# Performance work log

Measured on AMD Instinct MI355X. Metric: run time of the kernel, lower is better.

Reference implementation:

```python
import jax, jax.numpy as jnp
import numpy as np

N = 250_000   # nodes per graph batch
E = 4_000_000 # edges
G = 1024      # graphs (segments)
F_IN, C, D = 6, 64, 5
EPS = 1e-5    # PyG LayerNorm eps


def setup_inputs() -> dict:
    key = jax.random.key(0)
    ks = jax.random.split(key, 30)
    rn = lambda k, s: jax.random.normal(k, s, jnp.float32)
    p = lambda k, s: rn(k, s) * 0.05
    return {
        "x1": rn(ks[0], (N, F_IN)),
        "edge_index1": jax.random.randint(ks[1], (2, E), 0, N, jnp.int32),
        "batch1": jnp.sort(jax.random.randint(ks[2], (N,), 0, G, jnp.int32)),
        "x2": rn(ks[3], (N, F_IN)),
        "edge_index2": jax.random.randint(ks[4], (2, E), 0, N, jnp.int32),
        "batch2": jnp.sort(jax.random.randint(ks[5], (N,), 0, G, jnp.int32)),
        "d1": rn(ks[6], (G, D)),
        "d2": rn(ks[7], (G, D)),
        # GIN MLP 1: Linear(6,64) -> ReLU -> Linear(64,64)
        "W1": p(ks[8], (F_IN, C)), "b1": jnp.zeros((C,), jnp.float32),
        "W2": p(ks[9], (C, C)),    "b2": jnp.zeros((C,), jnp.float32),
        "ln1w": jnp.ones((C,), jnp.float32), "ln1b": jnp.zeros((C,), jnp.float32),
        # GIN MLP 2
        "W3": p(ks[10], (C, C)), "b3": jnp.zeros((C,), jnp.float32),
        "W4": p(ks[11], (C, C)), "b4": jnp.zeros((C,), jnp.float32),
        "ln2w": jnp.ones((C,), jnp.float32), "ln2b": jnp.zeros((C,), jnp.float32),
        # head: Linear(138,128) -> Linear(128,64) -> Linear(64,1)
        "Wf1": p(ks[12], (2 * C + 2 * D, 128)), "bf1": jnp.zeros((128,), jnp.float32),
        "Wf2": p(ks[13], (128, 64)),            "bf2": jnp.zeros((64,), jnp.float32),
        "Wo": p(ks[14], (64, 1)),               "bo": jnp.zeros((1,), jnp.float32),
    }


def _gin(x, src, dst, Wa, ba, Wb, bb):
    # GINConv, eps=0: h = x + sum_{j in N(i)} x_j ; then MLP (dropout = eval identity)
    agg = jax.ops.segment_sum(x[src], dst, num_segments=N)
    h = x + agg
    h = jax.nn.relu(h @ Wa + ba)
    return h @ Wb + bb


def _graph_layernorm(x, batch, w, b):
    # PyG LayerNorm mode='graph': normalize over all nodes AND channels per graph
    cnt = jax.ops.segment_sum(jnp.ones((x.shape[0],), x.dtype), batch, num_segments=G)
    norm = jnp.maximum(cnt, 1.0) * x.shape[-1]          # [G]
    mean = jax.ops.segment_sum(x.sum(-1), batch, num_segments=G) / norm
    xc = x - mean[batch][:, None]
    var = jax.ops.segment_sum((xc * xc).sum(-1), batch, num_segments=G) / norm
    out = xc * jax.lax.rsqrt(var + EPS)[batch][:, None]
    return out * w + b


def _forward_one(x, edge_index, batch, W1, b1, W2, b2, ln1w, ln1b, W3, b3, W4, b4, ln2w, ln2b):
    src, dst = edge_index[0], edge_index[1]
    x = jax.nn.relu(_graph_layernorm(_gin(x, src, dst, W1, b1, W2, b2), batch, ln1w, ln1b))
    x = jax.nn.relu(_graph_layernorm(_gin(x, src, dst, W3, b3, W4, b4), batch, ln2w, ln2b))
    add = jax.ops.segment_sum(x, batch, num_segments=G)  # [G, C]
    cnt = jax.ops.segment_sum(jnp.ones((x.shape[0],), x.dtype), batch, num_segments=G)
    mean = add / jnp.maximum(cnt, 1.0)[:, None]
    return add + mean


def reference(x1, edge_index1, batch1, x2, edge_index2, batch2, d1, d2,
              W1, b1, W2, b2, ln1w, ln1b, W3, b3, W4, b4, ln2w, ln2b,
              Wf1, bf1, Wf2, bf2, Wo, bo):
    shared = (W1, b1, W2, b2, ln1w, ln1b, W3, b3, W4, b4, ln2w, ln2b)
    emb1 = _forward_one(x1, edge_index1, batch1, *shared)
    emb2 = _forward_one(x2, edge_index2, batch2, *shared)
    h = jnp.concatenate([emb1, emb2, d1, d2], axis=1)    # [G, 138]
    h = jax.nn.relu(h @ Wf1 + bf1)                       # dropout identity (eval)
    h = jax.nn.relu(h @ Wf2 + bf2)
    return h @ Wo + bo                                   # [G, 1]
```

## Files before the change

### kernel.cpp

```cpp
#include <hip/hip_runtime.h>

typedef unsigned short ushort_t;
typedef __attribute__((ext_vector_type(8))) short bf16x8;
typedef __attribute__((ext_vector_type(4))) float f32x4;

#define FIN 6
#define CAP 20480

__device__ __forceinline__ float blo(unsigned u) { return __uint_as_float(u << 16); }
__device__ __forceinline__ float bhi(unsigned u) { return __uint_as_float(u & 0xffff0000u); }
__device__ __forceinline__ ushort_t f2b(float f) {
  unsigned u = __float_as_uint(f);
  unsigned r = (u + 0x7fffu + ((u >> 16) & 1u)) >> 16;
  return (ushort_t)r;
}
__device__ __forceinline__ float b2f(ushort_t s) { return __uint_as_float(((unsigned)s) << 16); }
__device__ __forceinline__ unsigned pk2(float lo, float hi) {
  return ((unsigned)f2b(hi) << 16) | (unsigned)f2b(lo);
}
union U4F { uint4 u; bf16x8 v; };
__device__ __forceinline__ bf16x8 asfrag(uint4 u) { U4F x; x.u = u; return x.v; }

#define EPT 32
#define TILE 8192

__global__ void k_binit(int* __restrict__ ecur, int* __restrict__ off, int nbuk, int N, int E) {
  int t = threadIdx.x;
  if (t < nbuk) ecur[t] = t * CAP;
  if (t == 0) off[N] = E;
}

__global__ __launch_bounds__(256) void k_bscatter(const int* __restrict__ src,
    const int* __restrict__ dst, int* __restrict__ ecur,
    unsigned* __restrict__ ebuf, int E, int nbuk) {
  __shared__ int cnt[256];
  __shared__ int gbase[256];
  int t = threadIdx.x;
  cnt[t] = 0;
  __syncthreads();
  int base = blockIdx.x * TILE;
  unsigned pk[EPT];
  unsigned pv[EPT];
  #pragma unroll
  for (int k = 0; k < EPT; ++k) {
    int e = base + k * 256 + t;
    if (e < E) {
      int d = dst[e];
      int b = d >> 10;
      int r = atomicAdd(&cnt[b], 1);
      pk[k] = (unsigned)b | ((unsigned)r << 8);
      pv[k] = ((unsigned)(d & 1023) << 18) | (unsigned)src[e];
    } else {
      pk[k] = 0xFFFFFFFFu;
    }
  }
  __syncthreads();
  if (t < nbuk && cnt[t] > 0) gbase[t] = atomicAdd(&ecur[t], cnt[t]);
  __syncthreads();
  #pragma unroll
  for (int k = 0; k < EPT; ++k) {
    if (pk[k] != 0xFFFFFFFFu) {
      int b = pk[k] & 255;
      int r = pk[k] >> 8;
      ebuf[gbase[b] + r] = pv[k];
    }
  }
}

__global__ __launch_bounds__(256) void k_bscan2(const int* __restrict__ ecur,
    int* __restrict__ ebase, int nbuk) {
  __shared__ int lds[256];
  int t = threadIdx.x;
  int s = (t < nbuk) ? (ecur[t] - t * CAP) : 0;
  lds[t] = s; __syncthreads();
  int acc = s;
  for (int o = 1; o < 256; o <<= 1) {
    int add = (t >= o) ? lds[t - o] : 0;
    __syncthreads();
    acc += add; lds[t] = acc;
    __syncthreads();
  }
  if (t < nbuk) ebase[t] = acc - s;
}

__global__ __launch_bounds__(256) void k_bcsr(const unsigned* __restrict__ ebuf,
    const int* __restrict__ ecur, const int* __restrict__ ebase,
    int* __restrict__ off, int* __restrict__ csr, int N) {
  __shared__ int hist[1024];
  __shared__ int lofs[1024];
  __shared__ int sc[256];
  int b = blockIdx.x, t = threadIdx.x;
  int nb0 = b << 10;
  int bn = N - nb0; if (bn > 1024) bn = 1024;
  int s_beg = b * CAP, s_end = ecur[b];
  int base = ebase[b];
  #pragma unroll
  for (int k = 0; k < 4; ++k) hist[t * 4 + k] = 0;
  __syncthreads();
  for (int e = s_beg + t; e < s_end; e += 256) atomicAdd(&hist[ebuf[e] >> 18], 1);
  __syncthreads();
  int h0 = hist[t * 4 + 0], h1 = hist[t * 4 + 1], h2 = hist[t * 4 + 2], h3 = hist[t * 4 + 3];
  int s = h0 + h1 + h2 + h3;
  sc[t] = s; __syncthreads();
  int acc = s;
  for (int o = 1; o < 256; o <<= 1) {
    int add = (t >= o) ? sc[t - o] : 0;
    __syncthreads();
    acc += add; sc[t] = acc;
    __syncthreads();
  }
  int run = acc - s;
  lofs[t * 4 + 0] = run; run += h0;
  lofs[t * 4 + 1] = run; run += h1;
  lofs[t * 4 + 2] = run; run += h2;
  lofs[t * 4 + 3] = run;
  __syncthreads();
  #pragma unroll
  for (int k = 0; k < 4; ++k) {
    int j = t * 4 + k;
    if (j < bn) off[nb0 + j] = base + lofs[j];
  }
  __syncthreads();
  for (int e = s_beg + t; e < s_end; e += 256) {
    unsigned p = ebuf[e];
    int r = atomicAdd(&lofs[p >> 18], 1);
    csr[base + r] = (int)(p & 0x3FFFFu);
  }
}

__global__ void k_bounds(const int* __restrict__ batch, int* __restrict__ gstart, int n, int G) {
  int i = blockIdx.x * 256 + threadIdx.x;
  if (i >= n) return;
  int b = batch[i];
  if (i == 0) { for (int g = 0; g <= b; ++g) gstart[g] = 0; }
  else { int pb = batch[i - 1]; for (int g = pb + 1; g <= b; ++g) gstart[g] = i; }
  if (i == n - 1) { for (int g = b + 1; g <= G; ++g) gstart[g] = n; }
}

__global__ void k_xpack(const float* __restrict__ x, unsigned* __restrict__ xb, int n) {
  int tt = blockIdx.x * 256 + threadIdx.x;
  if (tt >= n * 4) return;
  int i = tt >> 2, k = tt & 3;
  unsigned v = 0;
  if (k < 3) {
    float2 f = *(const float2*)(x + (size_t)i * 6 + k * 2);
    v = pk2(f.x, f.y);
  }
  xb[tt] = v;
}

__global__ void k_wpack(const float* __restrict__ W2, const float* __restrict__ W3,
                        const float* __restrict__ W4, uint4* __restrict__ wfrag) {
  int idx = blockIdx.x * 256 + threadIdx.x;
  if (idx >= 3 * 512) return;
  int widx = idx >> 9, rem = idx & 511;
  int mt = rem >> 7, kh = (rem >> 6) & 1, l = rem & 63;
  int g = l >> 4, c = l & 15;
  const float* W = (widx == 0) ? W2 : (widx == 1) ? W3 : W4;
  int k0 = kh * 32 + g * 8;
  int col = mt * 16 + c;
  uint4 v;
  v.x = pk2(W[(k0 + 0) * 64 + col], W[(k0 + 1) * 64 + col]);
  v.y = pk2(W[(k0 + 2) * 64 + col], W[(k0 + 3) * 64 + col]);
  v.z = pk2(W[(k0 + 4) * 64 + col], W[(k0 + 5) * 64 + col]);
  v.w = pk2(W[(k0 + 6) * 64 + col], W[(k0 + 7) * 64 + col]);
  wfrag[idx] = v;
}

#define ACC6(u) { a0 += blo(u.x); a1 += bhi(u.x); a2 += blo(u.y); a3 += bhi(u.y); a4 += blo(u.z); a5 += bhi(u.z); }
__global__ __launch_bounds__(256) void k_gin1a(const uint4* __restrict__ xb4,
    const int* __restrict__ off, const int* __restrict__ csr,
    const float* __restrict__ W1, const float* __restrict__ b1,
    ushort_t* __restrict__ t1, int n) {
  int t = threadIdx.x, w = t >> 6, lane = t & 63;
  int nd = lane >> 3, sl = lane & 7;
  int i = blockIdx.x * 32 + w * 8 + nd;

  float w1r[FIN];
  #pragma unroll
  for (int k = 0; k < FIN; ++k) w1r[k] = W1[k * 64 + lane];
  float bb1 = b1[lane];

  float a0 = 0, a1 = 0, a2 = 0, a3 = 0, a4 = 0, a5 = 0;
  if (i < n) {
    int e0 = off[i], e1 = off[i + 1];
    int e = e0 + sl;
    for (; e + 8 < e1; e += 16) {
      uint4 u = xb4[csr[e]];
      uint4 v = xb4[csr[e + 8]];
      ACC6(u); ACC6(v);
    }
    if (e < e1) { uint4 u = xb4[csr[e]]; ACC6(u); }
    if (sl == 0) { uint4 u = xb4[i]; ACC6(u); }
  }
  #pragma unroll
  for (int m = 1; m < 8; m <<= 1) {
    a0 += __shfl_xor(a0, m); a1 += __shfl_xor(a1, m); a2 += __shfl_xor(a2, m);
    a3 += __shfl_xor(a3, m); a4 += __shfl_xor(a4, m); a5 += __shfl_xor(a5, m);
  }
  __shared__ float sh[4][8][FIN];
  if (sl < FIN) {
    float v = (sl == 0) ? a0 : (sl == 1) ? a1 : (sl == 2) ? a2 : (sl == 3) ? a3 : (sl == 4) ? a4 : a5;
    sh[w][nd][sl] = v;
  }
  #pragma unroll
  for (int nd2 = 0; nd2 < 8; ++nd2) {
    int node = blockIdx.x * 32 + w * 8 + nd2;
    if (node >= n) break;
    float h = bb1;
    #pragma unroll
    for (int k = 0; k < FIN; ++k) h = fmaf(sh[w][nd2][k], w1r[k], h);
    t1[(size_t)node * 64 + lane] = f2b(fmaxf(h, 0.f));
  }
}

__global__ __launch_bounds__(256) void k_lin_mfma(const ushort_t* __restrict__ in,
    const uint4* __restrict__ wf, const float* __restrict__ bias,
    ushort_t* __restrict__ out, int n) {
  __shared__ __align__(16) ushort_t lds[4][16][72];
  int t = threadIdx.x, w = t >> 6, l = t & 63;
  int g = l >> 4, c = l & 15;
  bf16x8 af[4][2];
  #pragma unroll
  for (int mt = 0; mt < 4; ++mt)
    #pragma unroll
    for (int kh = 0; kh < 2; ++kh) af[mt][kh] = asfrag(wf[(mt * 2 + kh) * 64 + l]);
  float bs[4][4];
  #pragma unroll
  for (int mt = 0; mt < 4; ++mt)
    #pragma unroll
    for (int r = 0; r < 4; ++r) bs[mt][r] = bias[mt * 16 + 4 * g + r];

  int ntile = (n + 15) >> 4;
  for (int tau = blockIdx.x * 4 + w; tau < ntile; tau += gridDim.x * 4) {
    int nb = tau << 4;
    int row = nb + c; if (row >= n) row = n - 1;
    const uint4* rp = (const uint4*)(in + (size_t)row * 64);
    bf16x8 bf0 = asfrag(rp[g]);
    bf16x8 bf1 = asfrag(rp[g + 4]);
    f32x4 acc[4];
    #pragma unroll
    for (int mt = 0; mt < 4; ++mt) {
      acc[mt] = (f32x4){bs[mt][0], bs[mt][1], bs[mt][2], bs[mt][3]};
      acc[mt] = __builtin_amdgcn_mfma_f32_16x16x32_bf16(af[mt][0], bf0, acc[mt], 0, 0, 0);
      acc[mt] = __builtin_amdgcn_mfma_f32_16x16x32_bf16(af[mt][1], bf1, acc[mt], 0, 0, 0);
    }
    #pragma unroll
    for (int mt = 0; mt < 4; ++mt) {
      uint2 pv;
      pv.x = pk2(acc[mt][0], acc[mt][1]);
      pv.y = pk2(acc[mt][2], acc[mt][3]);
      *(uint2*)&lds[w][c][mt * 16 + 4 * g] = pv;
    }
    int n2 = l >> 2, ch = (l & 3) * 16;
    uint4 s0 = *(const uint4*)&lds[w][n2][ch];
    uint4 s1 = *(const uint4*)&lds[w][n2][ch + 8];
    int orow = nb + n2;
    if (orow < n) {
      uint4* op = (uint4*)(out + (size_t)orow * 64);
      op[(l & 3) * 2] = s0;
      op[(l & 3) * 2 + 1] = s1;
    }
  }
}

__global__ __launch_bounds__(256) void k_mlp2_mfma(const ushort_t* __restrict__ aggb,
    const uint4* __restrict__ wf3, const float* __restrict__ b3,
    const uint4* __restrict__ wf4, const float* __restrict__ b4,
    ushort_t* __restrict__ zb, int n) {
  __shared__ __align__(16) ushort_t lds[4][16][72];
  int t = threadIdx.x, w = t >> 6, l = t & 63;
  int g = l >> 4, c = l & 15;
  bf16x8 a3[4][2], a4[4][2];
  #pragma unroll
  for (int mt = 0; mt < 4; ++mt)
    #pragma unroll
    for (int kh = 0; kh < 2; ++kh) {
      a3[mt][kh] = asfrag(wf3[(mt * 2 + kh) * 64 + l]);
      a4[mt][kh] = asfrag(wf4[(mt * 2 + kh) * 64 + l]);
    }
  float bs3[4][4], bs4[4][4];
  #pragma unroll
  for (int mt = 0; mt < 4; ++mt)
    #pragma unroll
    for (int r = 0; r < 4; ++r) {
      bs3[mt][r] = b3[mt * 16 + 4 * g + r];
      bs4[mt][r] = b4[mt * 16 + 4 * g + r];
    }

  int ntile = (n + 15) >> 4;
  for (int tau = blockIdx.x * 4 + w; tau < ntile; tau += gridDim.x * 4) {
    int nb = tau << 4;
    int row = nb + c; if (row >= n) row = n - 1;
    const uint4* rp = (const uint4*)(aggb + (size_t)row * 64);
    bf16x8 bf0 = asfrag(rp[g]);
    bf16x8 bf1 = asfrag(rp[g + 4]);
    f32x4 acc[4];
    #pragma unroll
    for (int mt = 0; mt < 4; ++mt) {
      acc[mt] = (f32x4){bs3[mt][0], bs3[mt][1], bs3[mt][2], bs3[mt][3]};
      acc[mt] = __builtin_amdgcn_mfma_f32_16x16x32_bf16(a3[mt][0], bf0, acc[mt], 0, 0, 0);
      acc[mt] = __builtin_amdgcn_mfma_f32_16x16x32_bf16(a3[mt][1], bf1, acc[mt], 0, 0, 0);
    }
    #pragma unroll
    for (int mt = 0; mt < 4; ++mt) {
      uint2 pv;
      pv.x = pk2(fmaxf(acc[mt][0], 0.f), fmaxf(acc[mt][1], 0.f));
      pv.y = pk2(fmaxf(acc[mt][2], 0.f), fmaxf(acc[mt][3], 0.f));
      *(uint2*)&lds[w][c][mt * 16 + 4 * g] = pv;
    }
    bf16x8 h0 = asfrag(*(const uint4*)&lds[w][c][8 * g]);
    bf16x8 h1 = asfrag(*(const uint4*)&lds[w][c][8 * g + 32]);
    f32x4 ac2[4];
    #pragma unroll
    for (int mt = 0; mt < 4; ++mt) {
      ac2[mt] = (f32x4){bs4[mt][0], bs4[mt][1], bs4[mt][2], bs4[mt][3]};
      ac2[mt] = __builtin_amdgcn_mfma_f32_16x16x32_bf16(a4[mt][0], h0, ac2[mt], 0, 0, 0);
      ac2[mt] = __builtin_amdgcn_mfma_f32_16x16x32_bf16(a4[mt][1], h1, ac2[mt], 0, 0, 0);
    }
    #pragma unroll
    for (int mt = 0; mt < 4; ++mt) {
      uint2 pv;
      pv.x = pk2(ac2[mt][0], ac2[mt][1]);
      pv.y = pk2(ac2[mt][2], ac2[mt][3]);
      *(uint2*)&lds[w][c][mt * 16 + 4 * g] = pv;
    }
    int n2 = l >> 2, ch = (l & 3) * 16;
    uint4 s0 = *(const uint4*)&lds[w][n2][ch];
    uint4 s1 = *(const uint4*)&lds[w][n2][ch + 8];
    int orow = nb + n2;
    if (orow < n) {
      uint4* op = (uint4*)(zb + (size_t)orow * 64);
      op[(l & 3) * 2] = s0;
      op[(l & 3) * 2 + 1] = s1;
    }
  }
}

#define ACC8(u) { a0 += blo(u.x); a1 += bhi(u.x); a2 += blo(u.y); a3 += bhi(u.y); \
                  a4 += blo(u.z); a5 += bhi(u.z); a6 += blo(u.w); a7 += bhi(u.w); }
__global__ __launch_bounds__(256) void k_agg64(const ushort_t* __restrict__ hb,
    const int* __restrict__ off, const int* __restrict__ csr,
    ushort_t* __restrict__ aggb, int n) {
  int t = threadIdx.x, w = t >> 6, lane = t & 63;
  int i = blockIdx.x * 4 + w;
  if (i >= n) return;
  int grp = lane >> 3, sl = lane & 7;
  int e0 = off[i], e1 = off[i + 1];
  const uint4* hb4 = (const uint4*)hb;
  float a0 = 0, a1 = 0, a2 = 0, a3 = 0, a4 = 0, a5 = 0, a6 = 0, a7 = 0;
  int e = e0 + grp;
  for (; e + 8 < e1; e += 16) {
    int sa = csr[e], sb = csr[e + 8];
    uint4 ua = hb4[(size_t)sa * 8 + sl];
    uint4 ub = hb4[(size_t)sb * 8 + sl];
    ACC8(ua); ACC8(ub);
  }
  if (e < e1) {
    int sa = csr[e];
    uint4 ua = hb4[(size_t)sa * 8 + sl];
    ACC8(ua);
  }
  #pragma unroll
  for (int m = 8; m < 64; m <<= 1) {
    a0 += __shfl_xor(a0, m); a1 += __shfl_xor(a1, m); a2 += __shfl_xor(a2, m);
    a3 += __shfl_xor(a3, m); a4 += __shfl_xor(a4, m); a5 += __shfl_xor(a5, m);
    a6 += __shfl_xor(a6, m); a7 += __shfl_xor(a7, m);
  }
  if (grp == 0) {
    uint4 us = hb4[(size_t)i * 8 + sl];
    ACC8(us);
    uint4 o;
    o.x = pk2(a0, a1); o.y = pk2(a2, a3); o.z = pk2(a4, a5); o.w = pk2(a6, a7);
    ((uint4*)aggb)[(size_t)i * 8 + sl] = o;
  }
}

__global__ __launch_bounds__(256) void k_ln_statsb(const ushort_t* __restrict__ h,
    const int* __restrict__ gstart, float* __restrict__ gmean, float* __restrict__ ginv) {
  int g = blockIdx.x;
  int s0 = gstart[g], s1 = gstart[g + 1];
  const uint2* p2 = (const uint2*)h;
  size_t j0 = (size_t)s0 * 16, j1 = (size_t)s1 * 16;
  float s = 0.f, ss = 0.f;
  for (size_t j = j0 + threadIdx.x; j < j1; j += 256) {
    uint2 u = p2[j];
    float v0 = blo(u.x), v1 = bhi(u.x), v2 = blo(u.y), v3 = bhi(u.y);
    s += (v0 + v1) + (v2 + v3);
    ss += v0 * v0 + v1 * v1 + v2 * v2 + v3 * v3;
  }
  __shared__ float l1[256], l2[256];
  l1[threadIdx.x] = s; l2[threadIdx.x] = ss;
  __syncthreads();
  for (int o = 128; o > 0; o >>= 1) {
    if (threadIdx.x < o) { l1[threadIdx.x] += l1[threadIdx.x + o]; l2[threadIdx.x] += l2[threadIdx.x + o]; }
    __syncthreads();
  }
  if (threadIdx.x == 0) {
    float cnt = (float)(s1 - s0);
    float norm = fmaxf(cnt, 1.f) * 64.f;
    float mean = l1[0] / norm;
    float var = l2[0] / norm - mean * mean;
    var = fmaxf(var, 0.f);
    gmean[g] = mean;
    ginv[g] = rsqrtf(var + 1e-5f);
  }
}

__global__ void k_ln_apply_relu(const ushort_t* __restrict__ hr, const int* __restrict__ batch,
    const float* __restrict__ gmean, const float* __restrict__ ginv,
    const float* __restrict__ w, const float* __restrict__ bb,
    ushort_t* __restrict__ hb, int n) {
  int tt = blockIdx.x * 256 + threadIdx.x;
  if (tt >= n * 8) return;
  int i = tt >> 3, q = tt & 7;
  int g = batch[i];
  float mean = gmean[g], inv = ginv[g];
  uint4 u = ((const uint4*)hr)[tt];
  float4 w0 = *(const float4*)(w + q * 8);
  float4 w1 = *(const float4*)(w + q * 8 + 4);
  float4 c0 = *(const float4*)(bb + q * 8);
  float4 c1 = *(const float4*)(bb + q * 8 + 4);
  uint4 o;
  o.x = pk2(fmaxf((blo(u.x) - mean) * inv * w0.x + c0.x, 0.f),
            fmaxf((bhi(u.x) - mean) * inv * w0.y + c0.y, 0.f));
  o.y = pk2(fmaxf((blo(u.y) - mean) * inv * w0.z + c0.z, 0.f),
            fmaxf((bhi(u.y) - mean) * inv * w0.w + c0.w, 0.f));
  o.z = pk2(fmaxf((blo(u.z) - mean) * inv * w1.x + c1.x, 0.f),
            fmaxf((bhi(u.z) - mean) * inv * w1.y + c1.y, 0.f));
  o.w = pk2(fmaxf((blo(u.w) - mean) * inv * w1.z + c1.z, 0.f),
            fmaxf((bhi(u.w) - mean) * inv * w1.w + c1.w, 0.f));
  ((uint4*)hb)[tt] = o;
}

__global__ __launch_bounds__(256) void k_pool(const ushort_t* __restrict__ zb,
    const int* __restrict__ gstart, const float* __restrict__ gmean, const float* __restrict__ ginv,
    const float* __restrict__ w, const float* __restrict__ bb, float* __restrict__ emb) {
  int g = blockIdx.x;
  int s0 = gstart[g], s1 = gstart[g + 1];
  int t = threadIdx.x, c2 = t & 31, sub = t >> 5;
  float mean = gmean[g], inv = ginv[g];
  float w0 = w[c2 * 2], w1 = w[c2 * 2 + 1], b0 = bb[c2 * 2], b1v = bb[c2 * 2 + 1];
  float acc0 = 0.f, acc1 = 0.f;
  const unsigned* zp = (const unsigned*)zb;
  for (int i = s0 + sub; i < s1; i += 8) {
    unsigned u = zp[(size_t)i * 32 + c2];
    acc0 += fmaxf((blo(u) - mean) * inv * w0 + b0, 0.f);
    acc1 += fmaxf((bhi(u) - mean) * inv * w1 + b1v, 0.f);
  }
  __shared__ float l0[256], l1[256];
  l0[t] = acc0; l1[t] = acc1;
  __syncthreads();
  if (sub == 0) {
    float t0 = 0.f, t1v = 0.f;
    #pragma unroll
    for (int s = 0; s < 8; ++s) { t0 += l0[s * 32 + c2]; t1v += l1[s * 32 + c2]; }
    float cnt = fmaxf((float)(s1 - s0), 1.f);
    emb[g * 64 + c2 * 2]     = t0 + t0 / cnt;
    emb[g * 64 + c2 * 2 + 1] = t1v + t1v / cnt;
  }
}

__global__ __launch_bounds__(128) void k_head(const float* __restrict__ emb1,
    const float* __restrict__ emb2, const float* __restrict__ d1, const float* __restrict__ d2,
    const float* __restrict__ Wf1, const float* __restrict__ bf1,
    const float* __restrict__ Wf2, const float* __restrict__ bf2,
    const float* __restrict__ Wo, const float* __restrict__ bo, float* __restrict__ out) {
  int g = blockIdx.x, t = threadIdx.x;
  __shared__ float v[138], h1s[128], h2s[64];
  if (t < 64) v[t] = emb1[g * 64 + t];
  else v[t] = emb2[g * 64 + (t - 64)];
  if (t < 5) v[128 + t] = d1[g * 5 + t];
  else if (t < 10) v[133 + (t - 5)] = d2[g * 5 + (t - 5)];
  __syncthreads();
  float a = bf1[t];
  for (int k = 0; k < 138; ++k) a = fmaf(v[k], Wf1[k * 128 + t], a);
  h1s[t] = fmaxf(a, 0.f);
  __syncthreads();
  if (t < 64) {
    float a2 = bf2[t];
    #pragma unroll 8
    for (int k = 0; k < 128; ++k) a2 = fmaf(h1s[k], Wf2[k * 64 + t], a2);
    h2s[t] = fmaxf(a2, 0.f);
  }
  __syncthreads();
  if (t == 0) {
    float s = bo[0];
    for (int k = 0; k < 64; ++k) s += h2s[k] * Wo[k];
    out[g] = s;
  }
}

extern "C" void kernel_launch(void* const* d_in, const int* in_sizes, int n_in,
                              void* d_out, int out_size, void* d_ws, size_t ws_size,
                              hipStream_t stream) {
  const float* x1     = (const float*)d_in[0];
  const int*   ei1    = (const int*)d_in[1];
  const int*   batch1 = (const int*)d_in[2];
  const float* x2     = (const float*)d_in[3];
  const int*   ei2    = (const int*)d_in[4];
  const int*   batch2 = (const int*)d_in[5];
  const float* d1     = (const float*)d_in[6];
  const float* d2     = (const float*)d_in[7];
  const float* W1  = (const float*)d_in[8],  *b1  = (const float*)d_in[9];
  const float* W2  = (const float*)d_in[10], *b2  = (const float*)d_in[11];
  const float* ln1w = (const float*)d_in[12], *ln1b = (const float*)d_in[13];
  const float* W3  = (const float*)d_in[14], *b3  = (const float*)d_in[15];
  const float* W4  = (const float*)d_in[16], *b4  = (const float*)d_in[17];
  const float* ln2w = (const float*)d_in[18], *ln2b = (const float*)d_in[19];
  const float* Wf1 = (const float*)d_in[20], *bf1 = (const float*)d_in[21];
  const float* Wf2 = (const float*)d_in[22], *bf2 = (const float*)d_in[23];
  const float* Wo  = (const float*)d_in[24], *bo  = (const float*)d_in[25];
  float* out = (float*)d_out;

  const int N = in_sizes[0] / FIN;
  const int G = in_sizes[6] / 5;
  const int E1 = in_sizes[1] / 2;
  const int E2 = in_sizes[4] / 2;
  const int Emax = (E1 > E2) ? E1 : E2;
  const int NBUK = (N + 1023) >> 10;

  char* p = (char*)d_ws;
  auto alloc = [&](size_t bytes) { void* r = p; p += (bytes + 255) & ~(size_t)255; return r; };
  int*      off    = (int*)alloc((size_t)(N + 1) * 4);
  int*      ecur   = (int*)alloc(256 * 4);
  int*      ebase  = (int*)alloc(257 * 4);
  int*      csr    = (int*)alloc((size_t)Emax * 4);
  int*      gstart = (int*)alloc((size_t)(G + 1) * 4);
  float*    gmean  = (float*)alloc((size_t)G * 4);
  float*    ginv   = (float*)alloc((size_t)G * 4);
  uint4*    wfrag  = (uint4*)alloc(3 * 512 * 16);
  unsigned* xb     = (unsigned*)alloc((size_t)N * 16);
  ushort_t* t1     = (ushort_t*)alloc((size_t)N * 64 * 2);
  ushort_t* hr     = (ushort_t*)alloc((size_t)N * 64 * 2);
  ushort_t* hb     = (ushort_t*)alloc((size_t)N * 64 * 2);
  float*    emb1   = (float*)alloc((size_t)G * 64 * 4);
  float*    emb2   = (float*)alloc((size_t)G * 64 * 4);
  ushort_t* aggb = t1;
  ushort_t* zb   = hr;
  unsigned* ebuf = (unsigned*)t1;

  const uint4* wf2 = wfrag;
  const uint4* wf3 = wfrag + 512;
  const uint4* wf4 = wfrag + 1024;

  const int GRID_N  = (N + 255) / 256;
  const int GRID_W  = (N + 3) / 4;
  const int GRID_G1 = (N + 31) / 32;
  const int GRID_A  = (N * 8 + 255) / 256;
  const int GRID_P  = (N * 4 + 255) / 256;

  k_wpack<<<6, 256, 0, stream>>>(W2, W3, W4, wfrag);

  auto run_graph = [&](const float* x, const int* ei, const int* batch, int E, float* emb) {
    const int* src = ei;
    const int* dst = ei + E;
    const int SCAT = (E + TILE - 1) / TILE;
    k_binit<<<1, 256, 0, stream>>>(ecur, off, NBUK, N, E);
    k_bscatter<<<SCAT, 256, 0, stream>>>(src, dst, ecur, ebuf, E, NBUK);
    k_bscan2<<<1, 256, 0, stream>>>(ecur, ebase, NBUK);
    k_bcsr<<<NBUK, 256, 0, stream>>>(ebuf, ecur, ebase, off, csr, N);
    k_bounds<<<GRID_N, 256, 0, stream>>>(batch, gstart, N, G);
    k_xpack<<<GRID_P, 256, 0, stream>>>(x, xb, N);

    k_gin1a<<<GRID_G1, 256, 0, stream>>>((const uint4*)xb, off, csr, W1, b1, t1, N);
    k_lin_mfma<<<2048, 256, 0, stream>>>(t1, wf2, b2, hr, N);
    k_ln_statsb<<<G, 256, 0, stream>>>(hr, gstart, gmean, ginv);
    k_ln_apply_relu<<<GRID_A, 256, 0, stream>>>(hr, batch, gmean, ginv, ln1w, ln1b, hb, N);
    k_agg64<<<GRID_W, 256, 0, stream>>>(hb, off, csr, aggb, N);
    k_mlp2_mfma<<<2048, 256, 0, stream>>>(aggb, wf3, b3, wf4, b4, zb, N);
    k_ln_statsb<<<G, 256, 0, stream>>>(zb, gstart, gmean, ginv);
    k_pool<<<G, 256, 0, stream>>>(zb, gstart, gmean, ginv, ln2w, ln2b, emb);
  };

  run_graph(x1, ei1, batch1, E1, emb1);
  run_graph(x2, ei2, batch2, E2, emb2);
  k_head<<<G, 128, 0, stream>>>(emb1, emb2, d1, d2, Wf1, bf1, Wf2, bf2, Wo, bo, out);
}
```

Baseline: 653.0 us.

## Fuse GIN first MLP, graph LayerNorm stats/apply, and pooling into fewer kernels

Merges the bounds and x-packing kernels, fuses the first GIN aggregation and its ReLU linear with the second linear via an LDS tile, and folds LayerNorm statistics together with the normalize pass (and with pooling for the second layer) into per-graph kernels that cache the graph's rows in LDS. This removes intermediate global round trips and several launches per graph. The per-graph LN kernels rely on graphs fitting LNCAP nodes in shared memory, fall back to global reloads otherwise, and use large LDS footprints that may reduce occupancy.

```diff
diff --git a/kernel.cpp b/kernel.cpp
--- a/kernel.cpp
+++ b/kernel.cpp
@@ -6,6 +6,7 @@
 
 #define FIN 6
 #define CAP 20480
+#define LNCAP 384
 
 __device__ __forceinline__ float blo(unsigned u) { return __uint_as_float(u << 16); }
 __device__ __forceinline__ float bhi(unsigned u) { return __uint_as_float(u & 0xffff0000u); }
@@ -128,25 +129,24 @@
   }
 }
 
-__global__ void k_bounds(const int* __restrict__ batch, int* __restrict__ gstart, int n, int G) {
-  int i = blockIdx.x * 256 + threadIdx.x;
-  if (i >= n) return;
-  int b = batch[i];
-  if (i == 0) { for (int g = 0; g <= b; ++g) gstart[g] = 0; }
-  else { int pb = batch[i - 1]; for (int g = pb + 1; g <= b; ++g) gstart[g] = i; }
-  if (i == n - 1) { for (int g = b + 1; g <= G; ++g) gstart[g] = n; }
-}
-
-__global__ void k_xpack(const float* __restrict__ x, unsigned* __restrict__ xb, int n) {
+__global__ void k_prep(const float* __restrict__ x, const int* __restrict__ batch,
+                       unsigned* __restrict__ xb, int* __restrict__ gstart, int n, int G) {
   int tt = blockIdx.x * 256 + threadIdx.x;
-  if (tt >= n * 4) return;
-  int i = tt >> 2, k = tt & 3;
-  unsigned v = 0;
-  if (k < 3) {
-    float2 f = *(const float2*)(x + (size_t)i * 6 + k * 2);
-    v = pk2(f.x, f.y);
-  }
-  xb[tt] = v;
+  if (tt < n * 4) {
+    int i = tt >> 2, k = tt & 3;
+    unsigned v = 0;
+    if (k < 3) {
+      float2 f = *(const float2*)(x + (size_t)i * 6 + k * 2);
+      v = pk2(f.x, f.y);
+    }
+    xb[tt] = v;
+  }
+  if (tt < n) {
+    int b = batch[tt];
+    if (tt == 0) { for (int g = 0; g <= b; ++g) gstart[g] = 0; }
+    else { int pb = batch[tt - 1]; for (int g = pb + 1; g <= b; ++g) gstart[g] = tt; }
+    if (tt == n - 1) { for (int g = b + 1; g <= G; ++g) gstart[g] = n; }
+  }
 }
 
 __global__ void k_wpack(const float* __restrict__ W2, const float* __restrict__ W3,
@@ -168,13 +168,17 @@
 }
 
 #define ACC6(u) { a0 += blo(u.x); a1 += bhi(u.x); a2 += blo(u.y); a3 += bhi(u.y); a4 += blo(u.z); a5 += bhi(u.z); }
-__global__ __launch_bounds__(256) void k_gin1a(const uint4* __restrict__ xb4,
+__global__ __launch_bounds__(256) void k_gin1f(const uint4* __restrict__ xb4,
     const int* __restrict__ off, const int* __restrict__ csr,
     const float* __restrict__ W1, const float* __restrict__ b1,
-    ushort_t* __restrict__ t1, int n) {
+    const uint4* __restrict__ wf2, const float* __restrict__ b2,
+    ushort_t* __restrict__ hr, int n) {
+  __shared__ __align__(16) ushort_t t1s[32][72];
+  __shared__ float sh[4][8][FIN];
   int t = threadIdx.x, w = t >> 6, lane = t & 63;
   int nd = lane >> 3, sl = lane & 7;
-  int i = blockIdx.x * 32 + w * 8 + nd;
+  int nb0 = blockIdx.x * 32;
+  int i = nb0 + w * 8 + nd;
 
   float w1r[FIN];
   #pragma unroll
@@ -198,50 +202,33 @@
     a0 += __shfl_xor(a0, m); a1 += __shfl_xor(a1, m); a2 += __shfl_xor(a2, m);
     a3 += __shfl_xor(a3, m); a4 += __shfl_xor(a4, m); a5 += __shfl_xor(a5, m);
   }
-  __shared__ float sh[4][8][FIN];
   if (sl < FIN) {
     float v = (sl == 0) ? a0 : (sl == 1) ? a1 : (sl == 2) ? a2 : (sl == 3) ? a3 : (sl == 4) ? a4 : a5;
     sh[w][nd][sl] = v;
   }
   #pragma unroll
   for (int nd2 = 0; nd2 < 8; ++nd2) {
-    int node = blockIdx.x * 32 + w * 8 + nd2;
-    if (node >= n) break;
     float h = bb1;
     #pragma unroll
     for (int k = 0; k < FIN; ++k) h = fmaf(sh[w][nd2][k], w1r[k], h);
-    t1[(size_t)node * 64 + lane] = f2b(fmaxf(h, 0.f));
-  }
-}
-
-__global__ __launch_bounds__(256) void k_lin_mfma(const ushort_t* __restrict__ in,
-    const uint4* __restrict__ wf, const float* __restrict__ bias,
-    ushort_t* __restrict__ out, int n) {
-  __shared__ __align__(16) ushort_t lds[4][16][72];
-  int t = threadIdx.x, w = t >> 6, l = t & 63;
-  int g = l >> 4, c = l & 15;
-  bf16x8 af[4][2];
-  #pragma unroll
-  for (int mt = 0; mt < 4; ++mt)
-    #pragma unroll
-    for (int kh = 0; kh < 2; ++kh) af[mt][kh] = asfrag(wf[(mt * 2 + kh) * 64 + l]);
-  float bs[4][4];
-  #pragma unroll
-  for (int mt = 0; mt < 4; ++mt)
-    #pragma unroll
-    for (int r = 0; r < 4; ++r) bs[mt][r] = bias[mt * 16 + 4 * g + r];
-
-  int ntile = (n + 15) >> 4;
-  for (int tau = blockIdx.x * 4 + w; tau < ntile; tau += gridDim.x * 4) {
-    int nb = tau << 4;
-    int row = nb + c; if (row >= n) row = n - 1;
-    const uint4* rp = (const uint4*)(in + (size_t)row * 64);
-    bf16x8 bf0 = asfrag(rp[g]);
-    bf16x8 bf1 = asfrag(rp[g + 4]);
+    t1s[w * 8 + nd2][lane] = f2b(fmaxf(h, 0.f));
+  }
+  __syncthreads();
+  if (w < 2) {
+    int g = lane >> 4, c = lane & 15;
+    bf16x8 af[4][2];
+    #pragma unroll
+    for (int mt = 0; mt < 4; ++mt)
+      #pragma unroll
+      for (int kh = 0; kh < 2; ++kh) af[mt][kh] = asfrag(wf2[(mt * 2 + kh) * 64 + lane]);
+    int r0 = w * 16 + c;
+    bf16x8 bf0 = asfrag(*(const uint4*)&t1s[r0][8 * g]);
+    bf16x8 bf1 = asfrag(*(const uint4*)&t1s[r0][8 * g + 32]);
     f32x4 acc[4];
     #pragma unroll
     for (int mt = 0; mt < 4; ++mt) {
-      acc[mt] = (f32x4){bs[mt][0], bs[mt][1], bs[mt][2], bs[mt][3]};
+      acc[mt] = (f32x4){b2[mt * 16 + 4 * g + 0], b2[mt * 16 + 4 * g + 1],
+                        b2[mt * 16 + 4 * g + 2], b2[mt * 16 + 4 * g + 3]};
       acc[mt] = __builtin_amdgcn_mfma_f32_16x16x32_bf16(af[mt][0], bf0, acc[mt], 0, 0, 0);
       acc[mt] = __builtin_amdgcn_mfma_f32_16x16x32_bf16(af[mt][1], bf1, acc[mt], 0, 0, 0);
     }
@@ -250,89 +237,16 @@
       uint2 pv;
       pv.x = pk2(acc[mt][0], acc[mt][1]);
       pv.y = pk2(acc[mt][2], acc[mt][3]);
-      *(uint2*)&lds[w][c][mt * 16 + 4 * g] = pv;
-    }
-    int n2 = l >> 2, ch = (l & 3) * 16;
-    uint4 s0 = *(const uint4*)&lds[w][n2][ch];
-    uint4 s1 = *(const uint4*)&lds[w][n2][ch + 8];
-    int orow = nb + n2;
+      *(uint2*)&t1s[r0][mt * 16 + 4 * g] = pv;
+    }
+    int n2 = lane >> 2, ch = (lane & 3) * 16;
+    uint4 s0 = *(const uint4*)&t1s[w * 16 + n2][ch];
+    uint4 s1 = *(const uint4*)&t1s[w * 16 + n2][ch + 8];
+    int orow = nb0 + w * 16 + n2;
     if (orow < n) {
-      uint4* op = (uint4*)(out + (size_t)orow * 64);
-      op[(l & 3) * 2] = s0;
-      op[(l & 3) * 2 + 1] = s1;
-    }
-  }
-}
-
-__global__ __launch_bounds__(256) void k_mlp2_mfma(const ushort_t* __restrict__ aggb,
-    const uint4* __restrict__ wf3, const float* __restrict__ b3,
-    const uint4* __restrict__ wf4, const float* __restrict__ b4,
-    ushort_t* __restrict__ zb, int n) {
-  __shared__ __align__(16) ushort_t lds[4][16][72];
-  int t = threadIdx.x, w = t >> 6, l = t & 63;
-  int g = l >> 4, c = l & 15;
-  bf16x8 a3[4][2], a4[4][2];
-  #pragma unroll
-  for (int mt = 0; mt < 4; ++mt)
-    #pragma unroll
-    for (int kh = 0; kh < 2; ++kh) {
-      a3[mt][kh] = asfrag(wf3[(mt * 2 + kh) * 64 + l]);
-      a4[mt][kh] = asfrag(wf4[(mt * 2 + kh) * 64 + l]);
-    }
-  float bs3[4][4], bs4[4][4];
-  #pragma unroll
-  for (int mt = 0; mt < 4; ++mt)
-    #pragma unroll
-    for (int r = 0; r < 4; ++r) {
-      bs3[mt][r] = b3[mt * 16 + 4 * g + r];
-      bs4[mt][r] = b4[mt * 16 + 4 * g + r];
-    }
-
-  int ntile = (n + 15) >> 4;
-  for (int tau = blockIdx.x * 4 + w; tau < ntile; tau += gridDim.x * 4) {
-    int nb = tau << 4;
-    int row = nb + c; if (row >= n) row = n - 1;
-    const uint4* rp = (const uint4*)(aggb + (size_t)row * 64);
-    bf16x8 bf0 = asfrag(rp[g]);
-    bf16x8 bf1 = asfrag(rp[g + 4]);
-    f32x4 acc[4];
-    #pragma unroll
-    for (int mt = 0; mt < 4; ++mt) {
-      acc[mt] = (f32x4){bs3[mt][0], bs3[mt][1], bs3[mt][2], bs3[mt][3]};
-      acc[mt] = __builtin_amdgcn_mfma_f32_16x16x32_bf16(a3[mt][0], bf0, acc[mt], 0, 0, 0);
-      acc[mt] = __builtin_amdgcn_mfma_f32_16x16x32_bf16(a3[mt][1], bf1, acc[mt], 0, 0, 0);
-    }
-    #pragma unroll
-    for (int mt = 0; mt < 4; ++mt) {
-      uint2 pv;
-      pv.x = pk2(fmaxf(acc[mt][0], 0.f), fmaxf(acc[mt][1], 0.f));
-      pv.y = pk2(fmaxf(acc[mt][2], 0.f), fmaxf(acc[mt][3], 0.f));
-      *(uint2*)&lds[w][c][mt * 16 + 4 * g] = pv;
-    }
-    bf16x8 h0 = asfrag(*(const uint4*)&lds[w][c][8 * g]);
-    bf16x8 h1 = asfrag(*(const uint4*)&lds[w][c][8 * g + 32]);
-    f32x4 ac2[4];
-    #pragma unroll
-    for (int mt = 0; mt < 4; ++mt) {
-      ac2[mt] = (f32x4){bs4[mt][0], bs4[mt][1], bs4[mt][2], bs4[mt][3]};
-      ac2[mt] = __builtin_amdgcn_mfma_f32_16x16x32_bf16(a4[mt][0], h0, ac2[mt], 0, 0, 0);
-      ac2[mt] = __builtin_amdgcn_mfma_f32_16x16x32_bf16(a4[mt][1], h1, ac2[mt], 0, 0, 0);
-    }
-    #pragma unroll
-    for (int mt = 0; mt < 4; ++mt) {
-      uint2 pv;
-      pv.x = pk2(ac2[mt][0], ac2[mt][1]);
-      pv.y = pk2(ac2[mt][2], ac2[mt][3]);
-      *(uint2*)&lds[w][c][mt * 16 + 4 * g] = pv;
-    }
-    int n2 = l >> 2, ch = (l & 3) * 16;
-    uint4 s0 = *(const uint4*)&lds[w][n2][ch];
-    uint4 s1 = *(const uint4*)&lds[w][n2][ch + 8];
-    int orow = nb + n2;
-    if (orow < n) {
-      uint4* op = (uint4*)(zb + (size_t)orow * 64);
-      op[(l & 3) * 2] = s0;
-      op[(l & 3) * 2 + 1] = s1;
+      uint4* op = (uint4*)(hr + (size_t)orow * 64);
+      op[(lane & 3) * 2] = s0;
+      op[(lane & 3) * 2 + 1] = s1;
     }
   }
 }
@@ -376,88 +290,186 @@
   }
 }
 
-__global__ __launch_bounds__(256) void k_ln_statsb(const ushort_t* __restrict__ h,
-    const int* __restrict__ gstart, float* __restrict__ gmean, float* __restrict__ ginv) {
-  int g = blockIdx.x;
-  int s0 = gstart[g], s1 = gstart[g + 1];
-  const uint2* p2 = (const uint2*)h;
-  size_t j0 = (size_t)s0 * 16, j1 = (size_t)s1 * 16;
+__global__ __launch_bounds__(256) void k_mlp2_mfma(const ushort_t* __restrict__ aggb,
+    const uint4* __restrict__ wf3, const float* __restrict__ b3,
+    const uint4* __restrict__ wf4, const float* __restrict__ b4,
+    ushort_t* __restrict__ zb, int n) {
+  __shared__ __align__(16) ushort_t lds[4][16][72];
+  int t = threadIdx.x, w = t >> 6, l = t & 63;
+  int g = l >> 4, c = l & 15;
+  bf16x8 a3[4][2], a4[4][2];
+  #pragma unroll
+  for (int mt = 0; mt < 4; ++mt)
+    #pragma unroll
+    for (int kh = 0; kh < 2; ++kh) {
+      a3[mt][kh] = asfrag(wf3[(mt * 2 + kh) * 64 + l]);
+      a4[mt][kh] = asfrag(wf4[(mt * 2 + kh) * 64 + l]);
+    }
+  float bs3[4][4], bs4[4][4];
+  #pragma unroll
+  for (int mt = 0; mt < 4; ++mt)
+    #pragma unroll
+    for (int r = 0; r < 4; ++r) {
+      bs3[mt][r] = b3[mt * 16 + 4 * g + r];
+      bs4[mt][r] = b4[mt * 16 + 4 * g + r];
+    }
+  int ntile = (n + 15) >> 4;
+  for (int tau = blockIdx.x * 4 + w; tau < ntile; tau += gridDim.x * 4) {
+    int nb = tau << 4;
+    int row = nb + c; if (row >= n) row = n - 1;
+    const uint4* rp = (const uint4*)(aggb + (size_t)row * 64);
+    bf16x8 bf0 = asfrag(rp[g]);
+    bf16x8 bf1 = asfrag(rp[g + 4]);
+    f32x4 acc[4];
+    #pragma unroll
+    for (int mt = 0; mt < 4; ++mt) {
+      acc[mt] = (f32x4){bs3[mt][0], bs3[mt][1], bs3[mt][2], bs3[mt][3]};
+      acc[mt] = __builtin_amdgcn_mfma_f32_16x16x32_bf16(a3[mt][0], bf0, acc[mt], 0, 0, 0);
+      acc[mt] = __builtin_amdgcn_mfma_f32_16x16x32_bf16(a3[mt][1], bf1, acc[mt], 0, 0, 0);
+    }
+    #pragma unroll
+    for (int mt = 0; mt < 4; ++mt) {
+      uint2 pv;
+      pv.x = pk2(fmaxf(acc[mt][0], 0.f), fmaxf(acc[mt][1], 0.f));
+      pv.y = pk2(fmaxf(acc[mt][2], 0.f), fmaxf(acc[mt][3], 0.f));
+      *(uint2*)&lds[w][c][mt * 16 + 4 * g] = pv;
+    }
+    bf16x8 h0 = asfrag(*(const uint4*)&lds[w][c][8 * g]);
+    bf16x8 h1 = asfrag(*(const uint4*)&lds[w][c][8 * g + 32]);
+    f32x4 ac2[4];
+    #pragma unroll
+    for (int mt = 0; mt < 4; ++mt) {
+      ac2[mt] = (f32x4){bs4[mt][0], bs4[mt][1], bs4[mt][2], bs4[mt][3]};
+      ac2[mt] = __builtin_amdgcn_mfma_f32_16x16x32_bf16(a4[mt][0], h0, ac2[mt], 0, 0, 0);
+      ac2[mt] = __builtin_amdgcn_mfma_f32_16x16x32_bf16(a4[mt][1], h1, ac2[mt], 0, 0, 0);
+    }
+    #pragma unroll
+    for (int mt = 0; mt < 4; ++mt) {
+      uint2 pv;
+      pv.x = pk2(ac2[mt][0], ac2[mt][1]);
+      pv.y = pk2(ac2[mt][2], ac2[mt][3]);
+      *(uint2*)&lds[w][c][mt * 16 + 4 * g] = pv;
+    }
+    int n2 = l >> 2, ch = (l & 3) * 16;
+    uint4 s0 = *(const uint4*)&lds[w][n2][ch];
+    uint4 s1 = *(const uint4*)&lds[w][n2][ch + 8];
+    int orow = nb + n2;
+    if (orow < n) {
+      uint4* op = (uint4*)(zb + (size_t)orow * 64);
+      op[(l & 3) * 2] = s0;
+      op[(l & 3) * 2 + 1] = s1;
+    }
+  }
+}
+
+__global__ __launch_bounds__(256) void k_ln1(const ushort_t* __restrict__ hr,
+    const int* __restrict__ gstart, const float* __restrict__ w, const float* __restrict__ bb,
+    ushort_t* __restrict__ hb) {
+  __shared__ uint4 st[LNCAP * 8];
+  __shared__ float l1[256], l2[256];
+  __shared__ float mm[2];
+  int g = blockIdx.x, t = threadIdx.x;
+  int s0 = gstart[g], s1 = gstart[g + 1], cnt = s1 - s0;
+  const uint4* src = (const uint4*)hr + (size_t)s0 * 8;
+  int nch = cnt * 8;
+  bool fit = cnt <= LNCAP;
   float s = 0.f, ss = 0.f;
-  for (size_t j = j0 + threadIdx.x; j < j1; j += 256) {
-    uint2 u = p2[j];
+  for (int j = t; j < nch; j += 256) {
+    uint4 u = src[j];
+    if (fit) st[j] = u;
     float v0 = blo(u.x), v1 = bhi(u.x), v2 = blo(u.y), v3 = bhi(u.y);
-    s += (v0 + v1) + (v2 + v3);
-    ss += v0 * v0 + v1 * v1 + v2 * v2 + v3 * v3;
-  }
+    float v4 = blo(u.z), v5 = bhi(u.z), v6 = blo(u.w), v7 = bhi(u.w);
+    s += ((v0 + v1) + (v2 + v3)) + ((v4 + v5) + (v6 + v7));
+    ss += ((v0 * v0 + v1 * v1) + (v2 * v2 + v3 * v3)) + ((v4 * v4 + v5 * v5) + (v6 * v6 + v7 * v7));
+  }
+  l1[t] = s; l2[t] = ss;
+  __syncthreads();
+  for (int o = 128; o > 0; o >>= 1) {
+    if (t < o) { l1[t] += l1[t + o]; l2[t] += l2[t + o]; }
+    __syncthreads();
+  }
+  if (t == 0) {
+    float cf = (float)cnt;
+    float norm = fmaxf(cf, 1.f) * 64.f;
+    float mean = l1[0] / norm;
+    float var = fmaxf(l2[0] / norm - mean * mean, 0.f);
+    mm[0] = mean; mm[1] = rsqrtf(var + 1e-5f);
+  }
+  __syncthreads();
+  float mean = mm[0], inv = mm[1];
+  uint4* dst = (uint4*)hb + (size_t)s0 * 8;
+  for (int j = t; j < nch; j += 256) {
+    uint4 u = fit ? st[j] : src[j];
+    int q = j & 7;
+    float4 w0 = *(const float4*)(w + q * 8);
+    float4 w1 = *(const float4*)(w + q * 8 + 4);
+    float4 c0 = *(const float4*)(bb + q * 8);
+    float4 c1 = *(const float4*)(bb + q * 8 + 4);
+    uint4 o;
+    o.x = pk2(fmaxf((blo(u.x) - mean) * inv * w0.x + c0.x, 0.f),
+              fmaxf((bhi(u.x) - mean) * inv * w0.y + c0.y, 0.f));
+    o.y = pk2(fmaxf((blo(u.y) - mean) * inv * w0.z + c0.z, 0.f),
+              fmaxf((bhi(u.y) - mean) * inv * w0.w + c0.w, 0.f));
+    o.z = pk2(fmaxf((blo(u.z) - mean) * inv * w1.x + c1.x, 0.f),
+              fmaxf((bhi(u.z) - mean) * inv * w1.y + c1.y, 0.f));
+    o.w = pk2(fmaxf((blo(u.w) - mean) * inv * w1.z + c1.z, 0.f),
+              fmaxf((bhi(u.w) - mean) * inv * w1.w + c1.w, 0.f));
+    dst[j] = o;
+  }
+}
+
+__global__ __launch_bounds__(256) void k_ln2pool(const ushort_t* __restrict__ zb,
+    const int* __restrict__ gstart, const float* __restrict__ w, const float* __restrict__ bb,
+    float* __restrict__ emb) {
+  __shared__ unsigned st[LNCAP * 32];
   __shared__ float l1[256], l2[256];
-  l1[threadIdx.x] = s; l2[threadIdx.x] = ss;
+  __shared__ float mm[2];
+  int g = blockIdx.x, t = threadIdx.x;
+  int s0 = gstart[g], s1 = gstart[g + 1], cnt = s1 - s0;
+  const unsigned* src = (const unsigned*)zb + (size_t)s0 * 32;
+  int nu = cnt * 32;
+  bool fit = cnt <= LNCAP;
+  float s = 0.f, ss = 0.f;
+  for (int j = t; j < nu; j += 256) {
+    unsigned u = src[j];
+    if (fit) st[j] = u;
+    float v0 = blo(u), v1 = bhi(u);
+    s += v0 + v1;
+    ss += v0 * v0 + v1 * v1;
+  }
+  l1[t] = s; l2[t] = ss;
   __syncthreads();
   for (int o = 128; o > 0; o >>= 1) {
-    if (threadIdx.x < o) { l1[threadIdx.x] += l1[threadIdx.x + o]; l2[threadIdx.x] += l2[threadIdx.x + o]; }
+    if (t < o) { l1[t] += l1[t + o]; l2[t] += l2[t + o]; }
     __syncthreads();
   }
-  if (threadIdx.x == 0) {
-    float cnt = (float)(s1 - s0);
-    float norm = fmaxf(cnt, 1.f) * 64.f;
+  if (t == 0) {
+    float cf = (float)cnt;
+    float norm = fmaxf(cf, 1.f) * 64.f;
     float mean = l1[0] / norm;
-    float var = l2[0] / norm - mean * mean;
-    var = fmaxf(var, 0.f);
-    gmean[g] = mean;
-    ginv[g] = rsqrtf(var + 1e-5f);
-  }
-}
-
-__global__ void k_ln_apply_relu(const ushort_t* __restrict__ hr, const int* __restrict__ batch,
-    const float* __restrict__ gmean, const float* __restrict__ ginv,
-    const float* __restrict__ w, const float* __restrict__ bb,
-    ushort_t* __restrict__ hb, int n) {
-  int tt = blockIdx.x * 256 + threadIdx.x;
-  if (tt >= n * 8) return;
-  int i = tt >> 3, q = tt & 7;
-  int g = batch[i];
-  float mean = gmean[g], inv = ginv[g];
-  uint4 u = ((const uint4*)hr)[tt];
-  float4 w0 = *(const float4*)(w + q * 8);
-  float4 w1 = *(const float4*)(w + q * 8 + 4);
-  float4 c0 = *(const float4*)(bb + q * 8);
-  float4 c1 = *(const float4*)(bb + q * 8 + 4);
-  uint4 o;
-  o.x = pk2(fmaxf((blo(u.x) - mean) * inv * w0.x + c0.x, 0.f),
-            fmaxf((bhi(u.x) - mean) * inv * w0.y + c0.y, 0.f));
-  o.y = pk2(fmaxf((blo(u.y) - mean) * inv * w0.z + c0.z, 0.f),
-            fmaxf((bhi(u.y) - mean) * inv * w0.w + c0.w, 0.f));
-  o.z = pk2(fmaxf((blo(u.z) - mean) * inv * w1.x + c1.x, 0.f),
-            fmaxf((bhi(u.z) - mean) * inv * w1.y + c1.y, 0.f));
-  o.w = pk2(fmaxf((blo(u.w) - mean) * inv * w1.z + c1.z, 0.f),
-            fmaxf((bhi(u.w) - mean) * inv * w1.w + c1.w, 0.f));
-  ((uint4*)hb)[tt] = o;
-}
-
-__global__ __launch_bounds__(256) void k_pool(const ushort_t* __restrict__ zb,
-    const int* __restrict__ gstart, const float* __restrict__ gmean, const float* __restrict__ ginv,
-    const float* __restrict__ w, const float* __restrict__ bb, float* __restrict__ emb) {
-  int g = blockIdx.x;
-  int s0 = gstart[g], s1 = gstart[g + 1];
-  int t = threadIdx.x, c2 = t & 31, sub = t >> 5;
-  float mean = gmean[g], inv = ginv[g];
+    float var = fmaxf(l2[0] / norm - mean * mean, 0.f);
+    mm[0] = mean; mm[1] = rsqrtf(var + 1e-5f);
+  }
+  __syncthreads();
+  float mean = mm[0], inv = mm[1];
+  int c2 = t & 31, sub = t >> 5;
   float w0 = w[c2 * 2], w1 = w[c2 * 2 + 1], b0 = bb[c2 * 2], b1v = bb[c2 * 2 + 1];
   float acc0 = 0.f, acc1 = 0.f;
-  const unsigned* zp = (const unsigned*)zb;
-  for (int i = s0 + sub; i < s1; i += 8) {
-    unsigned u = zp[(size_t)i * 32 + c2];
+  for (int i = sub; i < cnt; i += 8) {
+    unsigned u = fit ? st[i * 32 + c2] : src[(size_t)i * 32 + c2];
     acc0 += fmaxf((blo(u) - mean) * inv * w0 + b0, 0.f);
     acc1 += fmaxf((bhi(u) - mean) * inv * w1 + b1v, 0.f);
   }
-  __shared__ float l0[256], l1[256];
-  l0[t] = acc0; l1[t] = acc1;
+  __syncthreads();
+  l1[t] = acc0; l2[t] = acc1;
   __syncthreads();
   if (sub == 0) {
     float t0 = 0.f, t1v = 0.f;
     #pragma unroll
-    for (int s = 0; s < 8; ++s) { t0 += l0[s * 32 + c2]; t1v += l1[s * 32 + c2]; }
-    float cnt = fmaxf((float)(s1 - s0), 1.f);
-    emb[g * 64 + c2 * 2]     = t0 + t0 / cnt;
-    emb[g * 64 + c2 * 2 + 1] = t1v + t1v / cnt;
+    for (int sx = 0; sx < 8; ++sx) { t0 += l1[sx * 32 + c2]; t1v += l2[sx * 32 + c2]; }
+    float cf = fmaxf((float)cnt, 1.f);
+    emb[g * 64 + c2 * 2]     = t0 + t0 / cf;
+    emb[g * 64 + c2 * 2 + 1] = t1v + t1v / cf;
   }
 }
 
@@ -527,27 +539,22 @@
   int*      ebase  = (int*)alloc(257 * 4);
   int*      csr    = (int*)alloc((size_t)Emax * 4);
   int*      gstart = (int*)alloc((size_t)(G + 1) * 4);
-  float*    gmean  = (float*)alloc((size_t)G * 4);
-  float*    ginv   = (float*)alloc((size_t)G * 4);
   uint4*    wfrag  = (uint4*)alloc(3 * 512 * 16);
   unsigned* xb     = (unsigned*)alloc((size_t)N * 16);
-  ushort_t* t1     = (ushort_t*)alloc((size_t)N * 64 * 2);
   ushort_t* hr     = (ushort_t*)alloc((size_t)N * 64 * 2);
   ushort_t* hb     = (ushort_t*)alloc((size_t)N * 64 * 2);
   float*    emb1   = (float*)alloc((size_t)G * 64 * 4);
   float*    emb2   = (float*)alloc((size_t)G * 64 * 4);
-  ushort_t* aggb = t1;
-  ushort_t* zb   = hr;
-  unsigned* ebuf = (unsigned*)t1;
+  ushort_t* aggb = hr;
+  ushort_t* zb   = hb;
+  unsigned* ebuf = (unsigned*)hb;
 
   const uint4* wf2 = wfrag;
   const uint4* wf3 = wfrag + 512;
   const uint4* wf4 = wfrag + 1024;
 
-  const int GRID_N  = (N + 255) / 256;
   const int GRID_W  = (N + 3) / 4;
-  const int GRID_G1 = (N + 31) / 32;
-  const int GRID_A  = (N * 8 + 255) / 256;
+  const int GRID_F  = (N + 31) / 32;
   const int GRID_P  = (N * 4 + 255) / 256;
 
   k_wpack<<<6, 256, 0, stream>>>(W2, W3, W4, wfrag);
@@ -560,17 +567,13 @@
     k_bscatter<<<SCAT, 256, 0, stream>>>(src, dst, ecur, ebuf, E, NBUK);
     k_bscan2<<<1, 256, 0, stream>>>(ecur, ebase, NBUK);
     k_bcsr<<<NBUK, 256, 0, stream>>>(ebuf, ecur, ebase, off, csr, N);
-    k_bounds<<<GRID_N, 256, 0, stream>>>(batch, gstart, N, G);
-    k_xpack<<<GRID_P, 256, 0, stream>>>(x, xb, N);
-
-    k_gin1a<<<GRID_G1, 256, 0, stream>>>((const uint4*)xb, off, csr, W1, b1, t1, N);
-    k_lin_mfma<<<2048, 256, 0, stream>>>(t1, wf2, b2, hr, N);
-    k_ln_statsb<<<G, 256, 0, stream>>>(hr, gstart, gmean, ginv);
-    k_ln_apply_relu<<<GRID_A, 256, 0, stream>>>(hr, batch, gmean, ginv, ln1w, ln1b, hb, N);
+    k_prep<<<GRID_P, 256, 0, stream>>>(x, batch, xb, gstart, N, G);
+
+    k_gin1f<<<GRID_F, 256, 0, stream>>>((const uint4*)xb, off, csr, W1, b1, wf2, b2, hr, N);
+    k_ln1<<<G, 256, 0, stream>>>(hr, gstart, ln1w, ln1b, hb);
     k_agg64<<<GRID_W, 256, 0, stream>>>(hb, off, csr, aggb, N);
     k_mlp2_mfma<<<2048, 256, 0, stream>>>(aggb, wf3, b3, wf4, b4, zb, N);
-    k_ln_statsb<<<G, 256, 0, stream>>>(zb, gstart, gmean, ginv);
-    k_pool<<<G, 256, 0, stream>>>(zb, gstart, gmean, ginv, ln2w, ln2b, emb);
+    k_ln2pool<<<G, 256, 0, stream>>>(zb, gstart, ln2w, ln2b, emb);
   };
 
   run_graph(x1, ei1, batch1, E1, emb1);
```

Result: no change. 645.2 us (-1.2%).
